# Performance work log

Hardware: AMD Instinct MI355X
Metric: run time of the kernel (lower is better)

Reference implementation:

```python
import jax, jax.numpy as jnp
import numpy as np

N_NODES = 50000
N_EDGES = 800000
D = 64


def setup_inputs() -> dict:
    key = jax.random.key(0)
    k1, k2, k3, k4, k5 = jax.random.split(key, 5)
    x = jax.random.normal(k1, (N_NODES, D), dtype=jnp.float32)
    edge_index = jax.random.randint(k2, (2, N_EDGES), 0, N_NODES, dtype=jnp.int64)
    edge_weight = jax.random.uniform(k3, (N_EDGES,), dtype=jnp.float32)
    W = jax.random.normal(k4, (D, D), dtype=jnp.float32) / np.sqrt(D)
    b = jax.random.normal(k5, (D,), dtype=jnp.float32) * 0.01
    return {"x": x, "edge_index": edge_index, "edge_weight": edge_weight, "W": W, "b": b}


def reference(x, edge_index, edge_weight, W, b):
    # GCNConv (PyG defaults): add self-loops (weight 1), symmetric normalization,
    # linear transform then normalized scatter-add aggregation, bias, then ReLU.
    n = x.shape[0]
    loop = jnp.arange(n, dtype=edge_index.dtype)
    src = jnp.concatenate([edge_index[0], loop])          # [E+N] message sources
    dst = jnp.concatenate([edge_index[1], loop])          # [E+N] message targets
    ew = jnp.concatenate([edge_weight, jnp.ones((n,), dtype=x.dtype)])
    # degree on target nodes from edge weights
    deg = jax.ops.segment_sum(ew, dst, num_segments=n)
    dinv = jnp.where(deg > 0, jax.lax.rsqrt(deg), 0.0)
    norm = dinv[src] * ew * dinv[dst]                      # [E+N]
    h = x @ W                                              # [N, D] linear first
    msg = h[src] * norm[:, None]                           # gather + scale
    out = jax.ops.segment_sum(msg, dst, num_segments=n) + b
    return jax.nn.relu(out)
```

## Files before the change

kernel.cpp:

```cpp
#include <hip/hip_runtime.h>

#define N_NODES 50000
#define N_EDGES 800000
#define D 64
#define NBUCK 782
#define BINBLK 256
#define EPB 3125
#define ECHUNK 13
#define GEMMBLK ((N_NODES + 15) / 16)
#define CAP 1536
#define FIXSCALE 4194304.0f


__device__ inline unsigned short f2bf(float f) {
    unsigned u = __float_as_uint(f);
    unsigned r = (u + 0x7FFFu + ((u >> 16) & 1u)) >> 16;
    return (unsigned short)r;
}
__device__ inline float bf2f(unsigned short h) {
    return __uint_as_float(((unsigned)h) << 16);
}
__device__ inline int wave_incl_scan(int v, int lane) {
#pragma unroll
    for (int off = 1; off < 64; off <<= 1) {
        int n = __shfl_up(v, off, 64);
        if (lane >= off) v += n;
    }
    return v;
}


__global__ void k_zero(int* __restrict__ gcur) {
    int i = blockIdx.x * blockDim.x + threadIdx.x;
    if (i < NBUCK) gcur[i] = 0;
}

union ShU {
    int lh[NBUCK];
    struct { float Ws[D][D]; float Xs[4][D]; } gm;
};
__global__ __launch_bounds__(256) void k_bin_gemm(
        const int* __restrict__ src, const int* __restrict__ dst,
        const float* __restrict__ ew,
        int* __restrict__ gcur, unsigned long long* __restrict__ binned,
        const float* __restrict__ x, const float* __restrict__ W,
        unsigned short* __restrict__ hb) {
    __shared__ ShU sh;
    int t = threadIdx.x;
    if (blockIdx.x < BINBLK) {
        int* lh = sh.lh;
        for (int i = t; i < NBUCK; i += 256) lh[i] = 0;
        __syncthreads();
        int base = blockIdx.x * EPB;
#pragma unroll
        for (int i = 0; i < ECHUNK; ++i) {
            int k = i * 256 + t;
            if (k < EPB) atomicAdd(&lh[dst[base + k] >> 6], 1);
        }
        __syncthreads();
        for (int i = t; i < NBUCK; i += 256) {
            int c = lh[i];
            lh[i] = (c > 0) ? atomicAdd(&gcur[i], c) : 0;
        }
        __syncthreads();
#pragma unroll
        for (int i = 0; i < ECHUNK; ++i) {
            int k = i * 256 + t;
            if (k < EPB) {
                int e = base + k;
                int d = dst[e];
                int bkt = d >> 6;
                int pos = atomicAdd(&lh[bkt], 1);
                if (pos < CAP)
                    binned[(size_t)bkt * CAP + pos] =
                        ((unsigned long long)__float_as_uint(ew[e]) << 32)
                      | ((unsigned)src[e] << 16) | (unsigned)d;
            }
        }
    } else {
        float (*Ws)[D] = sh.gm.Ws;
        float (*Xs)[D] = sh.gm.Xs;
        for (int k = t; k < D * D; k += 256) Ws[k / D][k % D] = W[k];
        int base = (blockIdx.x - BINBLK) * 16;
        int r = t >> 6, c = t & 63;
        for (int g = 0; g < 4; ++g) {
            int row = base + g * 4 + r;
            __syncthreads();
            Xs[r][c] = (row < N_NODES) ? x[(size_t)row * D + c] : 0.0f;
            __syncthreads();
            float acc = 0.0f;
#pragma unroll
            for (int k = 0; k < D; ++k) acc = fmaf(Xs[r][k], Ws[k][c], acc);
            if (row < N_NODES) hb[(size_t)row * D + c] = f2bf(acc);
        }
    }
}

__global__ void k_sortbucket(const unsigned long long* __restrict__ binned,
                             const int* __restrict__ gcur,
                             unsigned* __restrict__ csr,
                             unsigned* __restrict__ rc,
                             float* __restrict__ dinv) {
    __shared__ unsigned long long stage[CAP];
    __shared__ unsigned long long cw[64];
    __shared__ int off2[64];
    int t = threadIdx.x;
    if (t < 64) cw[t] = 0ULL;
    __syncthreads();
    int b = blockIdx.x;
    size_t beg = (size_t)b * CAP;
    int len = min(gcur[b], CAP);
    for (int k = t; k < len; k += 256) {
        unsigned long long p = binned[beg + k];
        stage[k] = p;
        int dl = (int)(p & 63);
        float w = __uint_as_float((unsigned)(p >> 32));
        atomicAdd(&cw[dl], (1ULL << 40) | (unsigned long long)__float2uint_rn(w * FIXSCALE));
    }
    __syncthreads();
    if (t < 64) {
        int c = (int)(cw[t] >> 40);
        float wfix = (float)(cw[t] & ((1ULL << 40) - 1ULL));
        int inc = wave_incl_scan(c, t);
        int excl = inc - c;
        off2[t] = excl;
        int node = b * 64 + t;
        if (node < N_NODES) {
            rc[node] = ((unsigned)c << 12) | (unsigned)excl;
            dinv[node] = rsqrtf(1.0f + wfix * (1.0f / FIXSCALE));
        }
    }
    __syncthreads();
    for (int k = t; k < len; k += 256) {
        unsigned long long p = stage[k];
        int dl = (int)(p & 63);
        int r = atomicAdd(&off2[dl], 1);
        unsigned short ewb = f2bf(__uint_as_float((unsigned)(p >> 32)));
        csr[beg + r] = ((unsigned)ewb << 16) | (unsigned)((p >> 16) & 0xffffu);
    }
}

__global__ void k_aggregate(const unsigned short* __restrict__ hb,
                            const float* __restrict__ dinv,
                            const unsigned* __restrict__ rc,
                            const unsigned* __restrict__ csr,
                            const float* __restrict__ bias,
                            float* __restrict__ out) {
    int node = blockIdx.x * 4 + (threadIdx.x >> 6);
    int lane = threadIdx.x & 63;
    if (node >= N_NODES) return;
    int half = lane >> 5;
    int cl = lane & 31;
    float di = dinv[node];
    unsigned r = rc[node];
    int cnt = (int)(r >> 12);
    size_t beg = (size_t)(node >> 6) * CAP + (r & 0xFFFu);
    float a0 = 0.0f, a1 = 0.0f, p0 = 0.0f, p1 = 0.0f;
    {
        unsigned hd = *(const unsigned*)(hb + (size_t)node * D + 2 * cl);
        float m = (half == 0) ? di : 0.0f;
        a0 = m * bf2f((unsigned short)hd);
        a1 = m * bf2f((unsigned short)(hd >> 16));
    }
    for (int b0 = 0; b0 < cnt; b0 += 64) {
        int n = min(64, cnt - b0);
        int my_src = 0;
        float my_ew = 0.0f;
        if (lane < n) {
            unsigned q = csr[beg + b0 + lane];
            my_src = (int)(q & 0xffffu);
            my_ew = bf2f((unsigned short)(q >> 16)) * dinv[my_src];
        }
        int jp = 0;
        for (; jp + 3 < n; jp += 4) {
            int iA = jp + half, iB = jp + 2 + half;
            int sA = __shfl(my_src, iA, 64);
            float eA = __shfl(my_ew, iA, 64);
            int sB = __shfl(my_src, iB, 64);
            float eB = __shfl(my_ew, iB, 64);
            unsigned hA = *(const unsigned*)(hb + (size_t)sA * D + 2 * cl);
            unsigned hB = *(const unsigned*)(hb + (size_t)sB * D + 2 * cl);
            a0 = fmaf(bf2f((unsigned short)hA), eA, a0);
            a1 = fmaf(bf2f((unsigned short)(hA >> 16)), eA, a1);
            p0 = fmaf(bf2f((unsigned short)hB), eB, p0);
            p1 = fmaf(bf2f((unsigned short)(hB >> 16)), eB, p1);
        }
        for (; jp + 1 < n; jp += 2) {
            int iA = jp + half;
            int sA = __shfl(my_src, iA, 64);
            float eA = __shfl(my_ew, iA, 64);
            unsigned hA = *(const unsigned*)(hb + (size_t)sA * D + 2 * cl);
            a0 = fmaf(bf2f((unsigned short)hA), eA, a0);
            a1 = fmaf(bf2f((unsigned short)(hA >> 16)), eA, a1);
        }
        if (jp < n) {
            int sA = __shfl(my_src, jp, 64);
            float eA = __shfl(my_ew, jp, 64);
            unsigned hA = *(const unsigned*)(hb + (size_t)sA * D + 2 * cl);
            float m = (half == 0) ? eA : 0.0f;
            a0 = fmaf(bf2f((unsigned short)hA), m, a0);
            a1 = fmaf(bf2f((unsigned short)(hA >> 16)), m, a1);
        }
    }
    a0 += p0; a1 += p1;
    a0 += __shfl_xor(a0, 32, 64);
    a1 += __shfl_xor(a1, 32, 64);
    if (half == 0) {
        float v0 = fmaf(di, a0, bias[2 * cl]);
        float v1 = fmaf(di, a1, bias[2 * cl + 1]);
        float2 o;
        o.x = fmaxf(v0, 0.0f);
        o.y = fmaxf(v1, 0.0f);
        *(float2*)(out + (size_t)node * D + 2 * cl) = o;
    }
}


extern "C" void kernel_launch(void* const* d_in, const int* in_sizes, int n_in,
                              void* d_out, int out_size, void* d_ws, size_t ws_size,
                              hipStream_t stream) {
    const float* x  = (const float*)d_in[0];
    const int*   ei = (const int*)d_in[1];
    const float* ew = (const float*)d_in[2];
    const float* W  = (const float*)d_in[3];
    const float* b  = (const float*)d_in[4];
    float* out = (float*)d_out;

    const int* src = ei;
    const int* dst = ei + N_EDGES;

    unsigned long long* binned = (unsigned long long*)d_ws;
    unsigned* csr      = (unsigned*)(binned + (size_t)NBUCK * CAP);
    int*   gcur        = (int*)(csr + (size_t)NBUCK * CAP);
    unsigned* rc       = (unsigned*)(gcur + 1024);
    float* dinv        = (float*)(rc + 50048);
    unsigned short* hb = (unsigned short*)(dinv + 50048);

    dim3 blk(256);
    k_zero<<<4, blk, 0, stream>>>(gcur);
    k_bin_gemm<<<BINBLK + GEMMBLK, blk, 0, stream>>>(src, dst, ew, gcur, binned,
                                                     x, W, hb);
    k_sortbucket<<<NBUCK, blk, 0, stream>>>(binned, gcur, csr, rc, dinv);
    k_aggregate<<<(N_NODES + 3) / 4, blk, 0, stream>>>(hb, dinv, rc, csr, b, out);
}
```

Baseline: 76.32 us.

## Replace global-atomic bucket cursors with per-block fixed slots plus overflow list

The binning phase stops using a counting pass and global atomicAdd on per-bucket cursors. Each bin block now writes edges into fixed 16-entry slots per (bucket, block) and records per-block counts in a byte array. Entries beyond 16 go to a shared overflow buffer, and the k_zero launch is replaced by a memset. The sort kernel prefix-scans the 256 per-block counts to compact the slots and then scans the whole overflow list for its bucket. This removes the histogram pass and global atomics, at the cost of sparser scattered reads and an overflow scan in every bucket block.

Result: slower. 84.34 us (+10.5%).

```diff
diff --git a/kernel.cpp b/kernel.cpp
--- a/kernel.cpp
+++ b/kernel.cpp
@@ -4,11 +4,13 @@
 #define N_EDGES 800000
 #define D 64
 #define NBUCK 782
+#define NBUCK_PAD 800
 #define BINBLK 256
 #define EPB 3125
 #define ECHUNK 13
-#define GEMMBLK ((N_NODES + 15) / 16)
+#define SLOTS 16
 #define CAP 1536
+#define OVFCAP 4096
 #define FIXSCALE 4194304.0f
 
 
@@ -29,11 +31,6 @@
     return v;
 }
 
-
-__global__ void k_zero(int* __restrict__ gcur) {
-    int i = blockIdx.x * blockDim.x + threadIdx.x;
-    if (i < NBUCK) gcur[i] = 0;
-}
 
 union ShU {
     int lh[NBUCK];
@@ -42,46 +39,44 @@
 __global__ __launch_bounds__(256) void k_bin_gemm(
         const int* __restrict__ src, const int* __restrict__ dst,
         const float* __restrict__ ew,
-        int* __restrict__ gcur, unsigned long long* __restrict__ binned,
+        unsigned long long* __restrict__ binned,
+        unsigned char* __restrict__ cnt8,
+        unsigned long long* __restrict__ ovf, int* __restrict__ ovfcnt,
         const float* __restrict__ x, const float* __restrict__ W,
         unsigned short* __restrict__ hb) {
     __shared__ ShU sh;
     int t = threadIdx.x;
-    if (blockIdx.x < BINBLK) {
+    int bid = blockIdx.x;
+    if (bid < BINBLK) {
         int* lh = sh.lh;
         for (int i = t; i < NBUCK; i += 256) lh[i] = 0;
         __syncthreads();
-        int base = blockIdx.x * EPB;
-#pragma unroll
-        for (int i = 0; i < ECHUNK; ++i) {
-            int k = i * 256 + t;
-            if (k < EPB) atomicAdd(&lh[dst[base + k] >> 6], 1);
-        }
-        __syncthreads();
-        for (int i = t; i < NBUCK; i += 256) {
-            int c = lh[i];
-            lh[i] = (c > 0) ? atomicAdd(&gcur[i], c) : 0;
-        }
-        __syncthreads();
+        int base = bid * EPB;
 #pragma unroll
         for (int i = 0; i < ECHUNK; ++i) {
             int k = i * 256 + t;
             if (k < EPB) {
                 int e = base + k;
                 int d = dst[e];
+                unsigned long long p =
+                    ((unsigned long long)__float_as_uint(ew[e]) << 32)
+                  | ((unsigned)src[e] << 16) | (unsigned)d;
                 int bkt = d >> 6;
-                int pos = atomicAdd(&lh[bkt], 1);
-                if (pos < CAP)
-                    binned[(size_t)bkt * CAP + pos] =
-                        ((unsigned long long)__float_as_uint(ew[e]) << 32)
-                      | ((unsigned)src[e] << 16) | (unsigned)d;
+                int rank = atomicAdd(&lh[bkt], 1);
+                if (rank < SLOTS)
+                    binned[((size_t)bkt * BINBLK + bid) * SLOTS + rank] = p;
+                else
+                    ovf[atomicAdd(ovfcnt, 1) & (OVFCAP - 1)] = p;
             }
         }
+        __syncthreads();
+        for (int i = t; i < NBUCK; i += 256)
+            cnt8[(size_t)bid * NBUCK_PAD + i] = (unsigned char)min(lh[i], SLOTS);
     } else {
         float (*Ws)[D] = sh.gm.Ws;
         float (*Xs)[D] = sh.gm.Xs;
         for (int k = t; k < D * D; k += 256) Ws[k / D][k % D] = W[k];
-        int base = (blockIdx.x - BINBLK) * 16;
+        int base = (bid - BINBLK) * 16;
         int r = t >> 6, c = t & 63;
         for (int g = 0; g < 4; ++g) {
             int row = base + g * 4 + r;
@@ -97,40 +92,72 @@
 }
 
 __global__ void k_sortbucket(const unsigned long long* __restrict__ binned,
-                             const int* __restrict__ gcur,
+                             const unsigned char* __restrict__ cnt8,
+                             const unsigned long long* __restrict__ ovf,
+                             const int* __restrict__ ovfcnt,
                              unsigned* __restrict__ csr,
                              unsigned* __restrict__ rc,
                              float* __restrict__ dinv) {
     __shared__ unsigned long long stage[CAP];
     __shared__ unsigned long long cw[64];
     __shared__ int off2[64];
-    int t = threadIdx.x;
+    __shared__ int wsum4[4];
+    __shared__ int lenSh;
+    int t = threadIdx.x, lane = t & 63, w = t >> 6;
     if (t < 64) cw[t] = 0ULL;
     __syncthreads();
     int b = blockIdx.x;
-    size_t beg = (size_t)b * CAP;
-    int len = min(gcur[b], CAP);
+    int c = (int)cnt8[(size_t)t * NBUCK_PAD + b];
+    int inc = wave_incl_scan(c, lane);
+    if (lane == 63) wsum4[w] = inc;
+    __syncthreads();
+    int woff = 0;
+#pragma unroll
+    for (int q = 0; q < 4; ++q) woff += (q < w) ? wsum4[q] : 0;
+    int off = inc - c + woff;
+    if (t == 255) lenSh = off + c;
+    __syncthreads();
+    {
+        size_t sbase = ((size_t)b * BINBLK + t) * SLOTS;
+        for (int j = 0; j < c; ++j) {
+            int pos = off + j;
+            if (pos < CAP) stage[pos] = binned[sbase + j];
+        }
+    }
+    __syncthreads();
+    {
+        int novf = min(*ovfcnt, OVFCAP);
+        for (int i = t; i < novf; i += 256) {
+            unsigned long long p = ovf[i];
+            if ((int)((p & 0xffffu) >> 6) == b) {
+                int pos = atomicAdd(&lenSh, 1);
+                if (pos < CAP) stage[pos] = p;
+            }
+        }
+    }
+    __syncthreads();
+    int len = min(lenSh, CAP);
     for (int k = t; k < len; k += 256) {
-        unsigned long long p = binned[beg + k];
-        stage[k] = p;
+        unsigned long long p = stage[k];
         int dl = (int)(p & 63);
-        float w = __uint_as_float((unsigned)(p >> 32));
-        atomicAdd(&cw[dl], (1ULL << 40) | (unsigned long long)__float2uint_rn(w * FIXSCALE));
+        float wg = __uint_as_float((unsigned)(p >> 32));
+        atomicAdd(&cw[dl], (1ULL << 40) | (unsigned long long)__float2uint_rn(wg * FIXSCALE));
     }
     __syncthreads();
     if (t < 64) {
-        int c = (int)(cw[t] >> 40);
+        int cc = (int)(cw[t] >> 40);
         float wfix = (float)(cw[t] & ((1ULL << 40) - 1ULL));
-        int inc = wave_incl_scan(c, t);
-        int excl = inc - c;
+        int inc2 = wave_incl_scan(cc, t);
+        int excl = inc2 - cc;
         off2[t] = excl;
         int node = b * 64 + t;
         if (node < N_NODES) {
-            rc[node] = ((unsigned)c << 12) | (unsigned)excl;
+            rc[node] = ((unsigned)cc << 12) | (unsigned)excl;
             dinv[node] = rsqrtf(1.0f + wfix * (1.0f / FIXSCALE));
         }
     }
     __syncthreads();
+    size_t beg = (size_t)b * CAP;
     for (int k = t; k < len; k += 256) {
         unsigned long long p = stage[k];
         int dl = (int)(p & 63);
@@ -230,16 +257,19 @@
     const int* dst = ei + N_EDGES;
 
     unsigned long long* binned = (unsigned long long*)d_ws;
-    unsigned* csr      = (unsigned*)(binned + (size_t)NBUCK * CAP);
-    int*   gcur        = (int*)(csr + (size_t)NBUCK * CAP);
-    unsigned* rc       = (unsigned*)(gcur + 1024);
+    unsigned long long* ovf = binned + (size_t)NBUCK * BINBLK * SLOTS;
+    unsigned* csr      = (unsigned*)(ovf + OVFCAP);
+    int*   ovfcnt      = (int*)(csr + (size_t)NBUCK * CAP);
+    unsigned* rc       = (unsigned*)(ovfcnt + 16);
     float* dinv        = (float*)(rc + 50048);
-    unsigned short* hb = (unsigned short*)(dinv + 50048);
+    unsigned char* cnt8 = (unsigned char*)(dinv + 50048);
+    unsigned short* hb = (unsigned short*)(cnt8 + (size_t)BINBLK * NBUCK_PAD);
 
     dim3 blk(256);
-    k_zero<<<4, blk, 0, stream>>>(gcur);
-    k_bin_gemm<<<BINBLK + GEMMBLK, blk, 0, stream>>>(src, dst, ew, gcur, binned,
-                                                     x, W, hb);
-    k_sortbucket<<<NBUCK, blk, 0, stream>>>(binned, gcur, csr, rc, dinv);
+    (void)hipMemsetAsync(ovfcnt, 0, sizeof(int), stream);
+    int gemmblk = (N_NODES + 15) / 16;
+    k_bin_gemm<<<BINBLK + gemmblk, blk, 0, stream>>>(src, dst, ew, binned, cnt8,
+                                                     ovf, ovfcnt, x, W, hb);
+    k_sortbucket<<<NBUCK, blk, 0, stream>>>(binned, cnt8, ovf, ovfcnt, csr, rc, dinv);
     k_aggregate<<<(N_NODES + 3) / 4, blk, 0, stream>>>(hb, dinv, rc, csr, b, out);
 }
```
